# Kernel tuning notes

Measured on AMD Instinct MI355X. Metric: run time of the kernel, lower is better.

The kernel has to match this reference:

```python
import jax, jax.numpy as jnp
import numpy as np

NUM_HEADS = 8
WS = 8          # window_size
MO = 12         # (1 + overlap) * window_size
PAD = 2         # overlap * window_size / 2


def setup_inputs() -> dict:
    key = jax.random.key(0)
    ks = jax.random.split(key, 5)
    B, C, H, W = 16, 256, 64, 64
    x = jax.random.normal(ks[0], (B, C, H, W), jnp.float32)
    W1 = jax.random.normal(ks[1], (3 * C, C), jnp.float32) * 0.02
    b1 = jnp.zeros((3 * C,), jnp.float32)
    W2 = jax.random.normal(ks[2], (C, C), jnp.float32) * 0.02
    b2 = jnp.zeros((C,), jnp.float32)
    return {"x": x, "W1": W1, "b1": b1, "W2": W2, "b2": b2}


def _unfold_windows(t, nwin):
    # t: (B, H, W, C) -> overlapping windows (B, nH, nwin, nwin, MO*MO, E)
    # Matches torch nn.Unfold(kernel=MO, stride=WS, padding=PAD) layout:
    # channels outermost, then kernel rows, then kernel cols.
    B, H, W, C = t.shape
    E = C // NUM_HEADS
    p = jnp.pad(t.transpose(0, 3, 1, 2), ((0, 0), (0, 0), (PAD, PAD), (PAD, PAD)))
    idx = (jnp.arange(nwin) * WS)[:, None] + jnp.arange(MO)  # (nwin, MO)
    g = p[:, :, idx]            # (B, C, nwin, MO, Wp)
    g = g[:, :, :, :, idx]      # (B, C, nwin, MO, nwin, MO)
    g = g.transpose(0, 1, 2, 4, 3, 5)            # (B, C, nwin, nwin, MO, MO)
    g = g.reshape(B, NUM_HEADS, E, nwin, nwin, MO * MO)
    return g.transpose(0, 1, 3, 4, 5, 2)         # (B, nH, nwin, nwin, MO^2, E)


def reference(x, W1, b1, W2, b2):
    B, C, H, W = x.shape
    E = C // NUM_HEADS
    nwin = H // WS
    t = x.transpose(0, 2, 3, 1)                  # (B, H, W, C)
    qkv = t @ W1.T + b1                          # (B, H, W, 3C)
    # '(c K)' layout with K=3: channel index outer, K inner -> strided split
    Q = qkv[..., 0::3]
    K = qkv[..., 1::3]
    V = qkv[..., 2::3]
    # Q -> non-overlapping windows: (B, nH, nwin, nwin, WS^2, E)
    Qw = Q.reshape(B, nwin, WS, nwin, WS, NUM_HEADS, E)
    Qw = Qw.transpose(0, 5, 1, 3, 2, 4, 6).reshape(B, NUM_HEADS, nwin, nwin, WS * WS, E)
    Kw = _unfold_windows(K, nwin)
    Vw = _unfold_windows(V, nwin)
    scale = 1.0 / jnp.sqrt(jnp.float32(E))
    scores = jnp.einsum('bhijqe,bhijke->bhijqk', Qw, Kw) * scale  # (B,nH,nw,nw,WS^2,MO^2)
    A = jax.nn.softmax(scores, axis=-1)
    out = jnp.einsum('bhijqk,bhijke->bhijqe', A, Vw)              # (B,nH,nw,nw,WS^2,E)
    out = out.reshape(B, NUM_HEADS, nwin, nwin, WS, WS, E)
    out = out.transpose(0, 2, 4, 3, 5, 1, 6).reshape(B, H, W, C)
    y = out @ W2.T + b2                                           # (B, H, W, C)
    return y.transpose(0, 3, 1, 2)                                # (B, C, H, W)
```

## Files before the change

kernel.cpp:

```cpp
#include <hip/hip_runtime.h>
#include <stdint.h>

typedef unsigned short u16;
typedef unsigned int   u32;
typedef __bf16 bf16x8_t __attribute__((ext_vector_type(8)));
typedef float  f32x4_t  __attribute__((ext_vector_type(4)));

#define MFMA16(a, b, c) __builtin_amdgcn_mfma_f32_16x16x32_bf16((a), (b), (c), 0, 0, 0)

__device__ __forceinline__ float bf2f(u16 u) {
    union { u32 i; float f; } c; c.i = ((u32)u) << 16; return c.f;
}
__device__ __forceinline__ u16 f2bf(float f) {
    union { float f; u32 i; } c; c.f = f;
    u32 x = c.i;
    return (u16)((x + 0x7fffu + ((x >> 16) & 1u)) >> 16);
}

__global__ __launch_bounds__(64) void detect_k(const u16* __restrict__ xu,
                                               u32* __restrict__ flag) {
    __shared__ int cnt;
    if (threadIdx.x == 0) cnt = 0;
    __syncthreads();
    int local = 0;
#pragma unroll
    for (int j = 0; j < 4; j++) {
        int i = threadIdx.x * 4 + j;
        u16 w = xu[2 * i];
        int e = (w >> 7) & 0xff;
        if (e >= 80 && e <= 160) local++;
    }
    atomicAdd(&cnt, local);
    __syncthreads();
    if (threadIdx.x == 0) *flag = (cnt < 160) ? 1u : 0u;
}

__global__ __launch_bounds__(256) void conv_w(const void* __restrict__ W1,
                                              const void* __restrict__ b1,
                                              const void* __restrict__ W2,
                                              const void* __restrict__ b2,
                                              const u32* __restrict__ flag,
                                              u16* __restrict__ W1b,
                                              u16* __restrict__ b1b,
                                              u16* __restrict__ W2b,
                                              u16* __restrict__ b2b) {
    int i = blockIdx.x * 256 + threadIdx.x;
    const int n1 = 196608, n2 = 768, n3 = 65536;
    const void* src; u16* dst; int li;
    if (i < n1)                { src = W1; dst = W1b; li = i; }
    else if (i < n1 + n2)      { src = b1; dst = b1b; li = i - n1; }
    else if (i < n1 + n2 + n3) { src = W2; dst = W2b; li = i - n1 - n2; }
    else                       { src = b2; dst = b2b; li = i - n1 - n2 - n3; }
    u16 v;
    if (*flag) v = f2bf(((const float*)src)[li]);
    else       v = ((const u16*)src)[li];
    dst[li] = v;
}

__global__ __launch_bounds__(256) void conv_x(const void* __restrict__ X,
                                              const u32* __restrict__ flag,
                                              u16* __restrict__ XT) {
    __shared__ __align__(16) u16 tile[64][68];
    const int b = blockIdx.z, c0 = blockIdx.y * 64, h0 = blockIdx.x * 64;
    const int tid = threadIdx.x;
    const int col = tid & 63, rq = tid >> 6;
    if (*flag) {
        const float* Xf = (const float*)X;
#pragma unroll
        for (int i = 0; i < 16; i++) {
            int row = i * 4 + rq;
            tile[row][col] = f2bf(Xf[((size_t)(b * 256 + c0 + row)) * 4096 + h0 + col]);
        }
    } else {
        const u16* Xh = (const u16*)X;
#pragma unroll
        for (int i = 0; i < 16; i++) {
            int row = i * 4 + rq;
            tile[row][col] = Xh[((size_t)(b * 256 + c0 + row)) * 4096 + h0 + col];
        }
    }
    __syncthreads();
#pragma unroll
    for (int i = 0; i < 16; i++) {
        int row = i * 4 + rq;
        XT[((size_t)(b * 4096 + h0 + row)) * 256 + c0 + col] = tile[col][row];
    }
}

__global__ __launch_bounds__(256) void gemm_qkv(const u16* __restrict__ XT,
                                                const u16* __restrict__ W1,
                                                const u16* __restrict__ b1,
                                                u16* __restrict__ Q2,
                                                u16* __restrict__ K2,
                                                u16* __restrict__ V2) {
    __shared__ __align__(16) u16 smem[128 * 64 + 96 * 64];
    u16* sA = smem;
    u16* sB = smem + 128 * 64;
    u16* Cs = smem;

    const int tid  = threadIdx.x;
    const int lane = tid & 63, wave = tid >> 6;
    const int quad = lane >> 4, l16 = lane & 15;
    const int wm = wave * 32;
    const int bm = blockIdx.x, h = blockIdx.y;
    const int o_base = h * 96;

    f32x4_t acc[2][6];
    const f32x4_t zz = {0.f, 0.f, 0.f, 0.f};
#pragma unroll
    for (int i = 0; i < 2; i++)
#pragma unroll
        for (int j = 0; j < 6; j++) acc[i][j] = zz;

    for (int kt = 0; kt < 256; kt += 64) {
        __syncthreads();
        uint4 av[4], bv[3];
#pragma unroll
        for (int i = 0; i < 4; i++) {
            int idx = i * 256 + tid;
            int row = idx >> 3, cp = idx & 7;
            av[i] = *(const uint4*)(XT + ((size_t)(bm * 128 + row)) * 256 + kt + cp * 8);
        }
#pragma unroll
        for (int i = 0; i < 3; i++) {
            int idx = i * 256 + tid;
            int row = idx >> 3, cp = idx & 7;
            bv[i] = *(const uint4*)(W1 + ((size_t)(o_base + row)) * 256 + kt + cp * 8);
        }
#pragma unroll
        for (int i = 0; i < 4; i++) {
            int idx = i * 256 + tid;
            int row = idx >> 3, cp = idx & 7;
            *(uint4*)(sA + row * 64 + ((cp ^ (row & 7)) * 8)) = av[i];
        }
#pragma unroll
        for (int i = 0; i < 3; i++) {
            int idx = i * 256 + tid;
            int row = idx >> 3, cp = idx & 7;
            *(uint4*)(sB + row * 64 + ((cp ^ (row & 7)) * 8)) = bv[i];
        }
        __syncthreads();
#pragma unroll
        for (int ks = 0; ks < 2; ks++) {
            bf16x8_t af[2], bg[6];
#pragma unroll
            for (int i = 0; i < 2; i++) {
                int row = wm + i * 16 + l16;
                int cp = (ks * 4 + quad) ^ (row & 7);
                af[i] = *(const bf16x8_t*)(sA + row * 64 + cp * 8);
            }
#pragma unroll
            for (int j = 0; j < 6; j++) {
                int row = j * 16 + l16;
                int cp = (ks * 4 + quad) ^ (row & 7);
                bg[j] = *(const bf16x8_t*)(sB + row * 64 + cp * 8);
            }
#pragma unroll
            for (int i = 0; i < 2; i++)
#pragma unroll
                for (int j = 0; j < 6; j++)
                    acc[i][j] = MFMA16(af[i], bg[j], acc[i][j]);
        }
    }

    __syncthreads();
#pragma unroll
    for (int j = 0; j < 6; j++) {
        float bias = bf2f(b1[o_base + j * 16 + l16]);
#pragma unroll
        for (int i = 0; i < 2; i++) {
            int m = wm + i * 16 + quad * 4;
#pragma unroll
            for (int r = 0; r < 4; r++)
                Cs[(m + r) * 104 + j * 16 + l16] = f2bf(acc[i][j][r] + bias);
        }
    }
    __syncthreads();

    const int b = bm >> 5;
    const int hw0 = (bm & 31) * 128;
    const size_t hb = ((size_t)(b * 8 + h)) * 4096;
#pragma unroll
    for (int it = 0; it < 2; it++) {
        int u = it * 256 + tid;
        int px = u >> 2, ch = u & 3;
        size_t gaddr = (hb + hw0 + px) * 32 + ch * 8;
#pragma unroll
        for (int w = 0; w < 3; w++) {
            u16 vals[8];
#pragma unroll
            for (int jj = 0; jj < 8; jj++)
                vals[jj] = Cs[px * 104 + 3 * (ch * 8 + jj) + w];
            uint4 pk;
            pk.x = (u32)vals[0] | ((u32)vals[1] << 16);
            pk.y = (u32)vals[2] | ((u32)vals[3] << 16);
            pk.z = (u32)vals[4] | ((u32)vals[5] << 16);
            pk.w = (u32)vals[6] | ((u32)vals[7] << 16);
            u16* dst = (w == 0) ? Q2 : (w == 1) ? K2 : V2;
            *(uint4*)(dst + gaddr) = pk;
        }
    }
}

__global__ __launch_bounds__(256) void attn_kernel(const u16* __restrict__ Q2,
                                                   const u16* __restrict__ K2,
                                                   const u16* __restrict__ V2,
                                                   u16* __restrict__ Op) {
    __shared__ __align__(16) u16 Qs[64 * 40];
    __shared__ __align__(16) u16 Ks[144 * 40];
    __shared__ __align__(16) u16 Vt[32 * 168];
    __shared__ __align__(16) u16 Ps[64 * 168];

    const int tid  = threadIdx.x;
    const int lane = tid & 63, wave = tid >> 6;
    const int quad = lane >> 4, l16 = lane & 15;
    const int win = blockIdx.x, head = blockIdx.y, b = blockIdx.z;
    const int wi = win >> 3, wj = win & 7;
    const size_t hb = ((size_t)(b * 8 + head)) * 4096;

    for (int t = tid; t < 64 * 16; t += 256) Ps[(t >> 4) * 168 + 144 + (t & 15)] = 0;
    for (int t = tid; t < 32 * 16; t += 256) Vt[(t >> 4) * 168 + 144 + (t & 15)] = 0;

    {
        int px = tid >> 2, ch = tid & 3;
        int qy = px >> 3, qx = px & 7;
        uint4 v = *(const uint4*)(Q2 + (hb + (wi * 8 + qy) * 64 + wj * 8 + qx) * 32 + ch * 8);
        *(uint4*)(Qs + px * 40 + ch * 8) = v;
    }
    for (int u = tid; u < 576; u += 256) {
        int px = u >> 2, ch = u & 3;
        int py = px / 12, kx = px - py * 12;
        int gy = wi * 8 - 2 + py, gx = wj * 8 - 2 + kx;
        uint4 v = make_uint4(0, 0, 0, 0);
        if (gy >= 0 && gy < 64 && gx >= 0 && gx < 64)
            v = *(const uint4*)(K2 + (hb + gy * 64 + gx) * 32 + ch * 8);
        *(uint4*)(Ks + px * 40 + ch * 8) = v;
    }
    for (int u = tid; u < 576; u += 256) {
        int px = u >> 2, ch = u & 3;
        int py = px / 12, kx = px - py * 12;
        int gy = wi * 8 - 2 + py, gx = wj * 8 - 2 + kx;
        uint4 v = make_uint4(0, 0, 0, 0);
        if (gy >= 0 && gy < 64 && gx >= 0 && gx < 64)
            v = *(const uint4*)(V2 + (hb + gy * 64 + gx) * 32 + ch * 8);
        int e0 = ch * 8;
        u32 vv[4] = {v.x, v.y, v.z, v.w};
#pragma unroll
        for (int p = 0; p < 4; p++) {
            Vt[(e0 + 2 * p    ) * 168 + px] = (u16)(vv[p] & 0xffff);
            Vt[(e0 + 2 * p + 1) * 168 + px] = (u16)(vv[p] >> 16);
        }
    }
    __syncthreads();

    const float scale = 0.17677669529663687f;
    float s[9][4];
    {
        bf16x8_t aF = *(const bf16x8_t*)(Qs + (wave * 16 + l16) * 40 + quad * 8);
        const f32x4_t zz = {0.f, 0.f, 0.f, 0.f};
#pragma unroll
        for (int j = 0; j < 9; j++) {
            bf16x8_t bF = *(const bf16x8_t*)(Ks + (j * 16 + l16) * 40 + quad * 8);
            f32x4_t d = MFMA16(aF, bF, zz);
#pragma unroll
            for (int r = 0; r < 4; r++) s[j][r] = d[r] * scale;
        }
    }
    float mx[4] = {-1e30f, -1e30f, -1e30f, -1e30f};
#pragma unroll
    for (int j = 0; j < 9; j++)
#pragma unroll
        for (int r = 0; r < 4; r++) mx[r] = fmaxf(mx[r], s[j][r]);
#pragma unroll
    for (int off = 1; off < 16; off <<= 1)
#pragma unroll
        for (int r = 0; r < 4; r++) mx[r] = fmaxf(mx[r], __shfl_xor(mx[r], off, 16));

    float sm[4] = {0.f, 0.f, 0.f, 0.f};
#pragma unroll
    for (int j = 0; j < 9; j++) {
#pragma unroll
        for (int r = 0; r < 4; r++) {
            float p = __expf(fminf(s[j][r] - mx[r], 0.f));
            u16 pb = f2bf(p);
            sm[r] += bf2f(pb);
            Ps[(wave * 16 + quad * 4 + r) * 168 + j * 16 + l16] = pb;
        }
    }
#pragma unroll
    for (int off = 1; off < 16; off <<= 1)
#pragma unroll
        for (int r = 0; r < 4; r++) sm[r] += __shfl_xor(sm[r], off, 16);

    __syncthreads();

    f32x4_t oa[2];
    oa[0] = (f32x4_t){0.f, 0.f, 0.f, 0.f};
    oa[1] = (f32x4_t){0.f, 0.f, 0.f, 0.f};
#pragma unroll
    for (int kk = 0; kk < 5; kk++) {
        bf16x8_t aP = *(const bf16x8_t*)(Ps + (wave * 16 + l16) * 168 + kk * 32 + quad * 8);
#pragma unroll
        for (int nt = 0; nt < 2; nt++) {
            bf16x8_t bV = *(const bf16x8_t*)(Vt + (nt * 16 + l16) * 168 + kk * 32 + quad * 8);
            oa[nt] = MFMA16(aP, bV, oa[nt]);
        }
    }
    float inv[4];
#pragma unroll
    for (int r = 0; r < 4; r++) inv[r] = 1.0f / fmaxf(sm[r], 1e-20f);
#pragma unroll
    for (int nt = 0; nt < 2; nt++) {
        int e = nt * 16 + l16;
#pragma unroll
        for (int r = 0; r < 4; r++) {
            int q = wave * 16 + quad * 4 + r;
            int qy = q >> 3, qx = q & 7;
            size_t pix = (size_t)(b * 4096) + (wi * 8 + qy) * 64 + (wj * 8 + qx);
            Op[pix * 256 + head * 32 + e] = f2bf(oa[nt][r] * inv[r]);
        }
    }
}

__device__ __forceinline__ void gemm_loop(const u16* __restrict__ A,
                                          const u16* __restrict__ B,
                                          int K, int bm, int bn,
                                          u16* sA, u16* sB, f32x4_t acc[4][4]) {
    const int tid  = threadIdx.x;
    const int lane = tid & 63, wave = tid >> 6;
    const int quad = lane >> 4, l16 = lane & 15;
    const int wm = (wave >> 1) * 64, wn = (wave & 1) * 64;

    for (int kt = 0; kt < K; kt += 64) {
        __syncthreads();
        uint4 av[4], bv[4];
#pragma unroll
        for (int i = 0; i < 4; i++) {
            int idx = i * 256 + tid;
            int row = idx >> 3, cp = idx & 7;
            av[i] = *(const uint4*)(A + ((size_t)(bm * 128 + row)) * K + kt + cp * 8);
            bv[i] = *(const uint4*)(B + ((size_t)(bn * 128 + row)) * K + kt + cp * 8);
        }
#pragma unroll
        for (int i = 0; i < 4; i++) {
            int idx = i * 256 + tid;
            int row = idx >> 3, cp = idx & 7;
            int sp = row * 64 + ((cp ^ (row & 7)) * 8);
            *(uint4*)(sA + sp) = av[i];
            *(uint4*)(sB + sp) = bv[i];
        }
        __syncthreads();
#pragma unroll
        for (int ks = 0; ks < 2; ks++) {
            bf16x8_t af[4], bg[4];
#pragma unroll
            for (int i = 0; i < 4; i++) {
                int row = wm + i * 16 + l16;
                int cp = (ks * 4 + quad) ^ (row & 7);
                af[i] = *(const bf16x8_t*)(sA + row * 64 + cp * 8);
            }
#pragma unroll
            for (int j = 0; j < 4; j++) {
                int row = wn + j * 16 + l16;
                int cp = (ks * 4 + quad) ^ (row & 7);
                bg[j] = *(const bf16x8_t*)(sB + row * 64 + cp * 8);
            }
#pragma unroll
            for (int i = 0; i < 4; i++)
#pragma unroll
                for (int j = 0; j < 4; j++)
                    acc[i][j] = MFMA16(af[i], bg[j], acc[i][j]);
        }
    }
}

__global__ __launch_bounds__(256) void gemm_out(const u16* __restrict__ Ap,
                                                const u16* __restrict__ W2,
                                                const u16* __restrict__ b2,
                                                const u32* __restrict__ flag,
                                                void* __restrict__ Y) {
    __shared__ __align__(16) u16 sA[128 * 64];
    __shared__ __align__(16) u16 sB[128 * 64];
    f32x4_t acc[4][4];
    const f32x4_t zz = {0.f, 0.f, 0.f, 0.f};
#pragma unroll
    for (int i = 0; i < 4; i++)
#pragma unroll
        for (int j = 0; j < 4; j++) acc[i][j] = zz;

    const int bm = blockIdx.x, bn = blockIdx.y;
    gemm_loop(Ap, W2, 256, bm, bn, sA, sB, acc);

    const int lane = threadIdx.x & 63, wave = threadIdx.x >> 6;
    const int quad = lane >> 4, l16 = lane & 15;
    const int wm = (wave >> 1) * 64, wn = (wave & 1) * 64;
    const int b = bm >> 5;
    const int hw0 = (bm & 31) * 128;
    const int out_f32 = (int)*flag;
#pragma unroll
    for (int j = 0; j < 4; j++) {
        int o = bn * 128 + wn + j * 16 + l16;
        float bias = bf2f(b2[o]);
        size_t base = ((size_t)(b * 256 + o)) * 4096;
        if (out_f32) {
            float* Yf = (float*)Y;
#pragma unroll
            for (int i = 0; i < 4; i++) {
                int m0 = hw0 + wm + i * 16 + quad * 4;
                f32x4_t ov;
#pragma unroll
                for (int r = 0; r < 4; r++) ov[r] = acc[i][j][r] + bias;
                *(f32x4_t*)(Yf + base + m0) = ov;
            }
        } else {
            u16* Yh = (u16*)Y;
#pragma unroll
            for (int i = 0; i < 4; i++) {
                int m0 = hw0 + wm + i * 16 + quad * 4;
                u32 lo = (u32)f2bf(acc[i][j][0] + bias) | ((u32)f2bf(acc[i][j][1] + bias) << 16);
                u32 hi = (u32)f2bf(acc[i][j][2] + bias) | ((u32)f2bf(acc[i][j][3] + bias) << 16);
                u32* d32 = (u32*)(Yh + base + m0);
                d32[0] = lo; d32[1] = hi;
            }
        }
    }
}

extern "C" void kernel_launch(void* const* d_in, const int* in_sizes, int n_in,
                              void* d_out, int out_size, void* d_ws, size_t ws_size,
                              hipStream_t stream) {
    (void)in_sizes; (void)n_in; (void)out_size; (void)ws_size;
    const void* x  = d_in[0];
    const void* W1 = d_in[1];
    const void* b1 = d_in[2];
    const void* W2 = d_in[3];
    const void* b2 = d_in[4];

    char* ws = (char*)d_ws;
    const size_t MB32 = (size_t)32 * 1024 * 1024;
    u16* xT  = (u16*)(ws);
    u16* Q2  = (u16*)(ws + MB32);
    u16* K2  = (u16*)(ws + 2 * MB32);
    u16* V2  = (u16*)(ws + 3 * MB32);
    u16* W1b = (u16*)(ws + 4 * MB32);
    u16* b1b = W1b + 196608;
    u16* W2b = b1b + 768;
    u16* b2b = W2b + 65536;
    u32* flag = (u32*)(b2b + 256);
    u16* Op  = xT;

    detect_k<<<1, 64, 0, stream>>>((const u16*)x, flag);
    conv_w  <<<1028, 256, 0, stream>>>(W1, b1, W2, b2, flag, W1b, b1b, W2b, b2b);
    conv_x  <<<dim3(64, 4, 16), 256, 0, stream>>>(x, flag, xT);
    gemm_qkv<<<dim3(512, 8), 256, 0, stream>>>(xT, W1b, b1b, Q2, K2, V2);
    attn_kernel<<<dim3(64, 8, 16), 256, 0, stream>>>(Q2, K2, V2, Op);
    gemm_out<<<dim3(512, 2), 256, 0, stream>>>(Op, W2b, b2b, flag, d_out);
}
```

Baseline: 277.9 us.

## Fuse dtype detection into kernels, swizzle GEMM grid, alias attention LDS

Removes the separate detect kernel and its global flag; every block of conv_w, conv_x and gemm_out now recomputes the fp32/bf16 check itself with a ballot over the first 256 elements. The QKV GEMM uses a 1D grid remapped so that groups of 8 row tiles share heads, which is meant to improve L2 reuse of the input and weights. The attention kernel aliases the P buffer onto K's shared memory, XOR-swizzles V-transpose stores to reduce LDS bank conflicts, merges the K and V loads into one loop, and folds the score scale into the exponent. Together these cut one launch and lower LDS usage, which may allow more blocks per CU, at the cost of redundant per-block detection work and an extra barrier.

```diff
diff --git a/kernel.cpp b/kernel.cpp
--- a/kernel.cpp
+++ b/kernel.cpp
@@ -17,33 +17,29 @@
     return (u16)((x + 0x7fffu + ((x >> 16) & 1u)) >> 16);
 }
 
-__global__ __launch_bounds__(64) void detect_k(const u16* __restrict__ xu,
-                                               u32* __restrict__ flag) {
-    __shared__ int cnt;
-    if (threadIdx.x == 0) cnt = 0;
-    __syncthreads();
-    int local = 0;
-#pragma unroll
-    for (int j = 0; j < 4; j++) {
-        int i = threadIdx.x * 4 + j;
-        u16 w = xu[2 * i];
-        int e = (w >> 7) & 0xff;
-        if (e >= 80 && e <= 160) local++;
-    }
-    atomicAdd(&cnt, local);
-    __syncthreads();
-    if (threadIdx.x == 0) *flag = (cnt < 160) ? 1u : 0u;
-}
-
-__global__ __launch_bounds__(256) void conv_w(const void* __restrict__ W1,
+__device__ __forceinline__ u32 detect_fp32(const u16* __restrict__ xu,
+                                           int tid, int* wcnt) {
+    u16 w = xu[2 * tid];
+    int e = (w >> 7) & 0xff;
+    int ok = (e >= 80 && e <= 160) ? 1 : 0;
+    unsigned long long m = __ballot(ok);
+    if ((tid & 63) == 0) wcnt[tid >> 6] = __popcll(m);
+    __syncthreads();
+    int cnt = wcnt[0] + wcnt[1] + wcnt[2] + wcnt[3];
+    return (cnt < 160) ? 1u : 0u;
+}
+
+__global__ __launch_bounds__(256) void conv_w(const u16* __restrict__ xu,
+                                              const void* __restrict__ W1,
                                               const void* __restrict__ b1,
                                               const void* __restrict__ W2,
                                               const void* __restrict__ b2,
-                                              const u32* __restrict__ flag,
                                               u16* __restrict__ W1b,
                                               u16* __restrict__ b1b,
                                               u16* __restrict__ W2b,
                                               u16* __restrict__ b2b) {
+    __shared__ int wcnt[4];
+    u32 f = detect_fp32(xu, threadIdx.x, wcnt);
     int i = blockIdx.x * 256 + threadIdx.x;
     const int n1 = 196608, n2 = 768, n3 = 65536;
     const void* src; u16* dst; int li;
@@ -52,19 +48,20 @@
     else if (i < n1 + n2 + n3) { src = W2; dst = W2b; li = i - n1 - n2; }
     else                       { src = b2; dst = b2b; li = i - n1 - n2 - n3; }
     u16 v;
-    if (*flag) v = f2bf(((const float*)src)[li]);
-    else       v = ((const u16*)src)[li];
+    if (f) v = f2bf(((const float*)src)[li]);
+    else   v = ((const u16*)src)[li];
     dst[li] = v;
 }
 
 __global__ __launch_bounds__(256) void conv_x(const void* __restrict__ X,
-                                              const u32* __restrict__ flag,
                                               u16* __restrict__ XT) {
     __shared__ __align__(16) u16 tile[64][68];
+    __shared__ int wcnt[4];
+    const int tid = threadIdx.x;
+    u32 f = detect_fp32((const u16*)X, tid, wcnt);
     const int b = blockIdx.z, c0 = blockIdx.y * 64, h0 = blockIdx.x * 64;
-    const int tid = threadIdx.x;
     const int col = tid & 63, rq = tid >> 6;
-    if (*flag) {
+    if (f) {
         const float* Xf = (const float*)X;
 #pragma unroll
         for (int i = 0; i < 16; i++) {
@@ -102,7 +99,9 @@
     const int lane = tid & 63, wave = tid >> 6;
     const int quad = lane >> 4, l16 = lane & 15;
     const int wm = wave * 32;
-    const int bm = blockIdx.x, h = blockIdx.y;
+    const int bx = blockIdx.x;
+    const int bm = (bx >> 6) * 8 + (bx & 7);
+    const int h  = (bx >> 3) & 7;
     const int o_base = h * 96;
 
     f32x4_t acc[2][6];
@@ -206,10 +205,11 @@
                                                    const u16* __restrict__ K2,
                                                    const u16* __restrict__ V2,
                                                    u16* __restrict__ Op) {
-    __shared__ __align__(16) u16 Qs[64 * 40];
-    __shared__ __align__(16) u16 Ks[144 * 40];
-    __shared__ __align__(16) u16 Vt[32 * 168];
-    __shared__ __align__(16) u16 Ps[64 * 168];
+    __shared__ __align__(16) u16 smem[18688];
+    u16* Qs = smem;
+    u16* Ks = smem + 2560;
+    u16* Ps = Ks;
+    u16* Vt = smem + 13312;
 
     const int tid  = threadIdx.x;
     const int lane = tid & 63, wave = tid >> 6;
@@ -218,9 +218,6 @@
     const int wi = win >> 3, wj = win & 7;
     const size_t hb = ((size_t)(b * 8 + head)) * 4096;
 
-    for (int t = tid; t < 64 * 16; t += 256) Ps[(t >> 4) * 168 + 144 + (t & 15)] = 0;
-    for (int t = tid; t < 32 * 16; t += 256) Vt[(t >> 4) * 168 + 144 + (t & 15)] = 0;
-
     {
         int px = tid >> 2, ch = tid & 3;
         int qy = px >> 3, qx = px & 7;
@@ -231,29 +228,28 @@
         int px = u >> 2, ch = u & 3;
         int py = px / 12, kx = px - py * 12;
         int gy = wi * 8 - 2 + py, gx = wj * 8 - 2 + kx;
-        uint4 v = make_uint4(0, 0, 0, 0);
-        if (gy >= 0 && gy < 64 && gx >= 0 && gx < 64)
-            v = *(const uint4*)(K2 + (hb + gy * 64 + gx) * 32 + ch * 8);
-        *(uint4*)(Ks + px * 40 + ch * 8) = v;
-    }
-    for (int u = tid; u < 576; u += 256) {
-        int px = u >> 2, ch = u & 3;
-        int py = px / 12, kx = px - py * 12;
-        int gy = wi * 8 - 2 + py, gx = wj * 8 - 2 + kx;
-        uint4 v = make_uint4(0, 0, 0, 0);
-        if (gy >= 0 && gy < 64 && gx >= 0 && gx < 64)
-            v = *(const uint4*)(V2 + (hb + gy * 64 + gx) * 32 + ch * 8);
+        uint4 kv = make_uint4(0, 0, 0, 0), vv = make_uint4(0, 0, 0, 0);
+        if (gy >= 0 && gy < 64 && gx >= 0 && gx < 64) {
+            size_t off = (hb + gy * 64 + gx) * 32 + ch * 8;
+            kv = *(const uint4*)(K2 + off);
+            vv = *(const uint4*)(V2 + off);
+        }
+        *(uint4*)(Ks + px * 40 + ch * 8) = kv;
+        int colp = px ^ (ch << 3);
         int e0 = ch * 8;
-        u32 vv[4] = {v.x, v.y, v.z, v.w};
+        u32 w0[4] = {vv.x, vv.y, vv.z, vv.w};
 #pragma unroll
         for (int p = 0; p < 4; p++) {
-            Vt[(e0 + 2 * p    ) * 168 + px] = (u16)(vv[p] & 0xffff);
-            Vt[(e0 + 2 * p + 1) * 168 + px] = (u16)(vv[p] >> 16);
-        }
-    }
-    __syncthreads();
-
-    const float scale = 0.17677669529663687f;
+            Vt[(e0 + 2 * p    ) * 168 + colp] = (u16)(w0[p] & 0xffff);
+            Vt[(e0 + 2 * p + 1) * 168 + colp] = (u16)(w0[p] >> 16);
+        }
+    }
+    for (int t = tid; t < 512; t += 256) {
+        int e = t >> 4, cl = 144 + (t & 15);
+        Vt[e * 168 + (cl ^ ((e >> 3) << 3))] = 0;
+    }
+    __syncthreads();
+
     float s[9][4];
     {
         bf16x8_t aF = *(const bf16x8_t*)(Qs + (wave * 16 + l16) * 40 + quad * 8);
@@ -263,7 +259,7 @@
             bf16x8_t bF = *(const bf16x8_t*)(Ks + (j * 16 + l16) * 40 + quad * 8);
             f32x4_t d = MFMA16(aF, bF, zz);
 #pragma unroll
-            for (int r = 0; r < 4; r++) s[j][r] = d[r] * scale;
+            for (int r = 0; r < 4; r++) s[j][r] = d[r];
         }
     }
     float mx[4] = {-1e30f, -1e30f, -1e30f, -1e30f};
@@ -276,15 +272,19 @@
 #pragma unroll
         for (int r = 0; r < 4; r++) mx[r] = fmaxf(mx[r], __shfl_xor(mx[r], off, 16));
 
+    __syncthreads();
+
+    *(unsigned long long*)(Ps + (wave * 16 + l16) * 168 + 144 + quad * 4) = 0ULL;
+
+    const float scale = 0.17677669529663687f;
     float sm[4] = {0.f, 0.f, 0.f, 0.f};
 #pragma unroll
     for (int j = 0; j < 9; j++) {
 #pragma unroll
         for (int r = 0; r < 4; r++) {
-            float p = __expf(fminf(s[j][r] - mx[r], 0.f));
-            u16 pb = f2bf(p);
-            sm[r] += bf2f(pb);
-            Ps[(wave * 16 + quad * 4 + r) * 168 + j * 16 + l16] = pb;
+            float p = __expf((s[j][r] - mx[r]) * scale);
+            sm[r] += p;
+            Ps[(wave * 16 + quad * 4 + r) * 168 + j * 16 + l16] = f2bf(p);
         }
     }
 #pragma unroll
@@ -302,13 +302,15 @@
         bf16x8_t aP = *(const bf16x8_t*)(Ps + (wave * 16 + l16) * 168 + kk * 32 + quad * 8);
 #pragma unroll
         for (int nt = 0; nt < 2; nt++) {
-            bf16x8_t bV = *(const bf16x8_t*)(Vt + (nt * 16 + l16) * 168 + kk * 32 + quad * 8);
+            int er = nt * 16 + l16;
+            int sw = (er >> 3) << 3;
+            bf16x8_t bV = *(const bf16x8_t*)(Vt + er * 168 + ((kk * 32 + quad * 8) ^ sw));
             oa[nt] = MFMA16(aP, bV, oa[nt]);
         }
     }
     float inv[4];
 #pragma unroll
-    for (int r = 0; r < 4; r++) inv[r] = 1.0f / fmaxf(sm[r], 1e-20f);
+    for (int r = 0; r < 4; r++) inv[r] = 1.0f / sm[r];
 #pragma unroll
     for (int nt = 0; nt < 2; nt++) {
         int e = nt * 16 + l16;
@@ -374,13 +376,16 @@
     }
 }
 
-__global__ __launch_bounds__(256) void gemm_out(const u16* __restrict__ Ap,
+__global__ __launch_bounds__(256) void gemm_out(const u16* __restrict__ xu,
+                                                const u16* __restrict__ Ap,
                                                 const u16* __restrict__ W2,
                                                 const u16* __restrict__ b2,
-                                                const u32* __restrict__ flag,
                                                 void* __restrict__ Y) {
     __shared__ __align__(16) u16 sA[128 * 64];
     __shared__ __align__(16) u16 sB[128 * 64];
+    __shared__ int wcnt[4];
+    const u32 out_f32 = detect_fp32(xu, threadIdx.x, wcnt);
+
     f32x4_t acc[4][4];
     const f32x4_t zz = {0.f, 0.f, 0.f, 0.f};
 #pragma unroll
@@ -396,7 +401,6 @@
     const int wm = (wave >> 1) * 64, wn = (wave & 1) * 64;
     const int b = bm >> 5;
     const int hw0 = (bm & 31) * 128;
-    const int out_f32 = (int)*flag;
 #pragma unroll
     for (int j = 0; j < 4; j++) {
         int o = bn * 128 + wn + j * 16 + l16;
@@ -435,6 +439,7 @@
     const void* b1 = d_in[2];
     const void* W2 = d_in[3];
     const void* b2 = d_in[4];
+    const u16* xu = (const u16*)x;
 
     char* ws = (char*)d_ws;
     const size_t MB32 = (size_t)32 * 1024 * 1024;
@@ -446,13 +451,11 @@
     u16* b1b = W1b + 196608;
     u16* W2b = b1b + 768;
     u16* b2b = W2b + 65536;
-    u32* flag = (u32*)(b2b + 256);
     u16* Op  = xT;
 
-    detect_k<<<1, 64, 0, stream>>>((const u16*)x, flag);
-    conv_w  <<<1028, 256, 0, stream>>>(W1, b1, W2, b2, flag, W1b, b1b, W2b, b2b);
-    conv_x  <<<dim3(64, 4, 16), 256, 0, stream>>>(x, flag, xT);
-    gemm_qkv<<<dim3(512, 8), 256, 0, stream>>>(xT, W1b, b1b, Q2, K2, V2);
+    conv_w  <<<1028, 256, 0, stream>>>(xu, W1, b1, W2, b2, W1b, b1b, W2b, b2b);
+    conv_x  <<<dim3(64, 4, 16), 256, 0, stream>>>(x, xT);
+    gemm_qkv<<<4096, 256, 0, stream>>>(xT, W1b, b1b, Q2, K2, V2);
     attn_kernel<<<dim3(64, 8, 16), 256, 0, stream>>>(Q2, K2, V2, Op);
-    gemm_out<<<dim3(512, 2), 256, 0, stream>>>(Op, W2b, b2b, flag, d_out);
-}
+    gemm_out<<<dim3(512, 2), 256, 0, stream>>>(xu, Op, W2b, b2b, d_out);
+}
```

New measurement: 242.7 us. 12.7% less time.
